# Performance work log

Measured on AMD Instinct MI355X. Metric: run time of the kernel, lower is better.

The kernel has to match this reference:

```python
import jax, jax.numpy as jnp
import numpy as np

RING_WORLD_SIZE = 4  # number of ring steps / KV sequence chunks


def _ring_flash_attention(q, k, v, ring_size):
    # q,k,v: [B, S, H, D]; non-causal full attention computed blockwise over
    # KV chunks (one per ring step) with numerically-stable online LSE merge,
    # mirroring _compact_ring_fwd + update_out_and_lse.
    B, S, H, D = q.shape
    scale = D ** (-0.5)
    chunk = S // ring_size
    out = None  # [B, S, H, D] accumulated in fp32
    lse = None  # [B, H, S] running log-sum-exp
    for step in range(ring_size):
        k_blk = jax.lax.dynamic_slice_in_dim(k, step * chunk, chunk, axis=1)
        v_blk = jax.lax.dynamic_slice_in_dim(v, step * chunk, chunk, axis=1)
        # scores: [B, H, Sq, Sk_blk]
        scores = jnp.einsum('bqhd,bkhd->bhqk', q, k_blk) * scale
        block_lse = jax.scipy.special.logsumexp(scores, axis=-1)  # [B,H,Sq]
        probs = jnp.exp(scores - block_lse[..., None])
        block_out = jnp.einsum('bhqk,bkhd->bqhd', probs, v_blk)
        if out is None:
            out, lse = block_out, block_lse
        else:
            new_lse = jnp.logaddexp(lse, block_lse)
            w_old = jnp.exp(lse - new_lse)       # [B,H,Sq]
            w_new = jnp.exp(block_lse - new_lse)
            # broadcast weights to [B,Sq,H,1]
            out = (jnp.transpose(w_old, (0, 2, 1))[..., None] * out
                   + jnp.transpose(w_new, (0, 2, 1))[..., None] * block_out)
            lse = new_lse
    return out.astype(q.dtype)


def setup_inputs() -> dict:
    key = jax.random.key(0)
    kq, kk, kv = jax.random.split(key, 3)
    shape = (1, 4096, 16, 128)
    return {
        'query': jax.random.normal(kq, shape, dtype=jnp.float32),
        'key': jax.random.normal(kk, shape, dtype=jnp.float32),
        'value': jax.random.normal(kv, shape, dtype=jnp.float32),
    }


def reference(query, key, value):
    # Ulysses all-to-all is identity on a single logical device; the ring loop
    # with lossless (error-feedback) KV compression reduces to blockwise
    # attention with online softmax merging.
    return _ring_flash_attention(query, key, value, RING_WORLD_SIZE)
```

## Files before the change

kernel.cpp:

```cpp
#include <hip/hip_runtime.h>
#include <hip/hip_bf16.h>

#define S_LEN 4096
#define NH    16
#define DD    128
#define HD    2048
#define QB    128
#define KB    64
#define NT    (S_LEN/KB)

typedef __bf16 bf16_t;
typedef bf16_t bf16x8 __attribute__((ext_vector_type(8)));
typedef float  f32x4  __attribute__((ext_vector_type(4)));

static __device__ __forceinline__ bf16x8 pack8(float4 a, float4 b, float s) {
  bf16x8 v;
  v[0]=(bf16_t)(a.x*s); v[1]=(bf16_t)(a.y*s); v[2]=(bf16_t)(a.z*s); v[3]=(bf16_t)(a.w*s);
  v[4]=(bf16_t)(b.x*s); v[5]=(bf16_t)(b.y*s); v[6]=(bf16_t)(b.z*s); v[7]=(bf16_t)(b.w*s);
  return v;
}

static __device__ __forceinline__ void gload_lds16(const void* g, void* l) {
  __builtin_amdgcn_global_load_lds((const __attribute__((address_space(1))) void*)g,
                                   (__attribute__((address_space(3))) void*)l, 16, 0, 0);
}

__global__ __launch_bounds__(256) void prep_k(const float* __restrict__ Kg,
                                              bf16_t* __restrict__ Kp) {
  const int kt = blockIdx.x, h = blockIdx.y, tid = threadIdx.x;
  __shared__ bf16_t tile[KB][DD + 8];
  #pragma unroll
  for (int it = 0; it < 8; ++it) {
    int lin4 = it*256 + tid;
    int r  = lin4 >> 5;
    int dc = (lin4 & 31) * 4;
    float4 a = *(const float4*)(Kg + (size_t)(kt*KB + r)*HD + h*DD + dc);
    tile[r][dc+0]=(bf16_t)a.x; tile[r][dc+1]=(bf16_t)a.y;
    tile[r][dc+2]=(bf16_t)a.z; tile[r][dc+3]=(bf16_t)a.w;
  }
  __syncthreads();
  bf16_t* out = Kp + (size_t)(h*NT + kt)*8192;
  #pragma unroll
  for (int it = 0; it < 4; ++it) {
    int cid = it*256 + tid;
    int f = cid >> 6, l = cid & 63;
    int b = f >> 2, c = f & 3;
    int row = b*16 + (l & 15);
    int d0  = c*32 + (l >> 4)*8;
    bf16x8 v = *(const bf16x8*)(&tile[row][d0]);
    *(bf16x8*)(out + (size_t)cid*8) = v;
  }
}

__global__ __launch_bounds__(256) void prep_v(const float* __restrict__ Vg,
                                              bf16_t* __restrict__ Vp) {
  const int kt = blockIdx.x, h = blockIdx.y, tid = threadIdx.x;
  __shared__ bf16_t tile[KB][DD + 8];
  #pragma unroll
  for (int it = 0; it < 8; ++it) {
    int lin4 = it*256 + tid;
    int r  = lin4 >> 5;
    int dc = (lin4 & 31) * 4;
    float4 a = *(const float4*)(Vg + (size_t)(kt*KB + r)*HD + h*DD + dc);
    tile[r][dc+0]=(bf16_t)a.x; tile[r][dc+1]=(bf16_t)a.y;
    tile[r][dc+2]=(bf16_t)a.z; tile[r][dc+3]=(bf16_t)a.w;
  }
  __syncthreads();
  bf16_t* out = Vp + (size_t)(h*NT + kt)*8192;
  #pragma unroll
  for (int it = 0; it < 4; ++it) {
    int cid = it*256 + tid;
    int f = cid >> 6, l = cid & 63;
    int ks = f >> 3, db = f & 7;
    int d  = db*16 + (l & 15);
    int c0 = ks*32 + (l >> 4)*8;
    bf16x8 v;
    #pragma unroll
    for (int m = 0; m < 8; ++m) {
      int c = c0 + m;
      int k = 32*(c>>5) + 16*((c>>2)&1) + 4*((c>>3)&3) + (c&3);
      v[m] = tile[k][d];
    }
    *(bf16x8*)(out + (size_t)cid*8) = v;
  }
}

__global__ __launch_bounds__(256, 2) void attn_fwd(const float* __restrict__ Qg,
                                                   const bf16_t* __restrict__ Kp,
                                                   const bf16_t* __restrict__ Vp,
                                                   float* __restrict__ Og) {
  const int phys = blockIdx.x;
  const int logical = (phys & 7) * 64 + (phys >> 3);
  const int h  = logical >> 5;
  const int qt = logical & 31;
  const int tid  = threadIdx.x;
  const int wid  = tid >> 6;
  const int lane = tid & 63;
  const int l16  = lane & 15;
  const int lg   = lane >> 4;
  const int lo16 = lane * 16;

  __shared__ alignas(16) bf16_t Ks[2][8192];
  __shared__ alignas(16) bf16_t Vt[2][8192];

  const float qs = 0.08838834764831845f * 1.4426950408889634f;
  bf16x8 qf[2][4];
  #pragma unroll
  for (int g = 0; g < 2; ++g) {
    const int qrow = qt*QB + wid*32 + g*16 + l16;
    const float* qp = Qg + (size_t)qrow*HD + h*DD + lg*8;
    #pragma unroll
    for (int c = 0; c < 4; ++c) {
      float4 a = *(const float4*)(qp + c*32);
      float4 b = *(const float4*)(qp + c*32 + 4);
      qf[g][c] = pack8(a, b, qs);
    }
  }
  bf16x8 onesf;
  #pragma unroll
  for (int j = 0; j < 8; ++j) onesf[j] = (bf16_t)1.0f;
  asm volatile("" ::: "memory");

  const int lo = tid*16;
  auto issue = [&](int kt) {
    int b = kt & 1;
    const char* kg = (const char*)(Kp + (size_t)(h*NT + kt)*8192);
    const char* vg = (const char*)(Vp + (size_t)(h*NT + kt)*8192);
    char* kl = (char*)&Ks[b][0];
    char* vl = (char*)&Vt[b][0];
    #pragma unroll
    for (int p = 0; p < 4; ++p) gload_lds16(kg + lo + p*4096, kl + lo + p*4096);
    #pragma unroll
    for (int p = 0; p < 4; ++p) gload_lds16(vg + lo + p*4096, vl + lo + p*4096);
  };

  f32x4 acc[2][8];
  f32x4 acc_l[2];
  #pragma unroll
  for (int g = 0; g < 2; ++g) {
    #pragma unroll
    for (int i = 0; i < 8; ++i) acc[g][i] = (f32x4){0.f,0.f,0.f,0.f};
    acc_l[g] = (f32x4){0.f,0.f,0.f,0.f};
  }
  float m_run[2] = {-__builtin_inff(), -__builtin_inff()};

  issue(0);
  issue(1);

  for (int kt = 0; kt < NT; ++kt) {
    if (kt == NT-1) { asm volatile("s_waitcnt vmcnt(0)" ::: "memory"); }
    else            { asm volatile("s_waitcnt vmcnt(8)" ::: "memory"); }
    __builtin_amdgcn_s_barrier();
    asm volatile("" ::: "memory");

    const int cur = kt & 1;
    const char* KsB = (const char*)&Ks[cur][0] + lo16;
    const char* VtB = (const char*)&Vt[cur][0] + lo16;

    f32x4 sc[2][4];
    #pragma unroll
    for (int g = 0; g < 2; ++g)
      #pragma unroll
      for (int b = 0; b < 4; ++b) sc[g][b] = (f32x4){0.f,0.f,0.f,0.f};
    __builtin_amdgcn_s_setprio(1);
    #pragma unroll
    for (int b = 0; b < 4; ++b) {
      #pragma unroll
      for (int c = 0; c < 4; ++c) {
        bf16x8 kb = *(const bf16x8*)(KsB + ((b*4 + c) << 10));
        sc[0][b] = __builtin_amdgcn_mfma_f32_16x16x32_bf16(kb, qf[0][c], sc[0][b], 0, 0, 0);
        sc[1][b] = __builtin_amdgcn_mfma_f32_16x16x32_bf16(kb, qf[1][c], sc[1][b], 0, 0, 0);
      }
    }
    __builtin_amdgcn_s_setprio(0);

    bf16x8 vf0[8], vf1[8];
    #pragma unroll
    for (int db = 0; db < 8; ++db) vf0[db] = *(const bf16x8*)(VtB + (db << 10));
    #pragma unroll
    for (int db = 0; db < 8; ++db) vf1[db] = *(const bf16x8*)(VtB + ((8 + db) << 10));

    bf16x8 pp[2][2];
    #pragma unroll
    for (int g = 0; g < 2; ++g) {
      float pmax;
      {
        float a0 = fmaxf(fmaxf(sc[g][0][0], sc[g][0][1]), sc[g][0][2]);
        float a1 = fmaxf(fmaxf(sc[g][0][3], sc[g][1][0]), sc[g][1][1]);
        float a2 = fmaxf(fmaxf(sc[g][1][2], sc[g][1][3]), sc[g][2][0]);
        float a3 = fmaxf(fmaxf(sc[g][2][1], sc[g][2][2]), sc[g][2][3]);
        float a4 = fmaxf(fmaxf(sc[g][3][0], sc[g][3][1]), sc[g][3][2]);
        float b0 = fmaxf(fmaxf(a0, a1), a2);
        float b1 = fmaxf(fmaxf(a3, a4), sc[g][3][3]);
        pmax = fmaxf(b0, b1);
        pmax = fmaxf(pmax, __shfl_xor(pmax, 16));
        pmax = fmaxf(pmax, __shfl_xor(pmax, 32));
      }
      if (!__all(pmax - m_run[g] <= 8.0f)) {
        float mnew  = fmaxf(m_run[g], pmax);
        float alpha = exp2f(m_run[g] - mnew);
        m_run[g] = mnew;
        #pragma unroll
        for (int i = 0; i < 8; ++i) {
          #pragma unroll
          for (int r = 0; r < 4; ++r) acc[g][i][r] *= alpha;
        }
        #pragma unroll
        for (int r = 0; r < 4; ++r) acc_l[g][r] *= alpha;
      }
      #pragma unroll
      for (int b = 0; b < 4; ++b) {
        #pragma unroll
        for (int r = 0; r < 4; ++r) {
          float p = exp2f(sc[g][b][r] - m_run[g]);
          pp[g][b >> 1][(b & 1)*4 + r] = (bf16_t)p;
        }
      }
    }

    __builtin_amdgcn_s_setprio(1);
    #pragma unroll
    for (int ks = 0; ks < 2; ++ks) {
      acc_l[0] = __builtin_amdgcn_mfma_f32_16x16x32_bf16(onesf, pp[0][ks], acc_l[0], 0, 0, 0);
      acc_l[1] = __builtin_amdgcn_mfma_f32_16x16x32_bf16(onesf, pp[1][ks], acc_l[1], 0, 0, 0);
      #pragma unroll
      for (int db = 0; db < 8; ++db) {
        bf16x8 va = ks ? vf1[db] : vf0[db];
        acc[0][db] = __builtin_amdgcn_mfma_f32_16x16x32_bf16(va, pp[0][ks], acc[0][db], 0, 0, 0);
        acc[1][db] = __builtin_amdgcn_mfma_f32_16x16x32_bf16(va, pp[1][ks], acc[1][db], 0, 0, 0);
      }
    }
    __builtin_amdgcn_s_setprio(0);

    __builtin_amdgcn_s_barrier();
    asm volatile("" ::: "memory");
    if (kt + 2 < NT) issue(kt + 2);
  }

  #pragma unroll
  for (int g = 0; g < 2; ++g) {
    const int qrow = qt*QB + wid*32 + g*16 + l16;
    const float inv = 1.0f / acc_l[g][0];
    float* op = Og + (size_t)qrow*HD + h*DD + lg*4;
    #pragma unroll
    for (int db = 0; db < 8; ++db) {
      float4 o;
      o.x = acc[g][db][0]*inv; o.y = acc[g][db][1]*inv;
      o.z = acc[g][db][2]*inv; o.w = acc[g][db][3]*inv;
      *(float4*)(op + db*16) = o;
    }
  }
}

extern "C" void kernel_launch(void* const* d_in, const int* in_sizes, int n_in,
                              void* d_out, int out_size, void* d_ws, size_t ws_size,
                              hipStream_t stream) {
  const float* Q = (const float*)d_in[0];
  const float* K = (const float*)d_in[1];
  const float* V = (const float*)d_in[2];
  float* O = (float*)d_out;
  bf16_t* Kp = (bf16_t*)d_ws;
  bf16_t* Vp = Kp + (size_t)NH*S_LEN*DD;
  prep_k<<<dim3(NT, NH), 256, 0, stream>>>(K, Kp);
  prep_v<<<dim3(NT, NH), 256, 0, stream>>>(V, Vp);
  attn_fwd<<<dim3(512), 256, 0, stream>>>(Q, Kp, Vp, O);
}
```

Baseline: 188.4 us.

## Software-pipeline QK^T of next tile with softmax and PV of current tile

Restructures the main loop so the QK^T MFMAs for tile kt+1 are computed before the softmax and PV of tile kt, with a prologue and an epilogue. The V fragments are loaded into registers before a barrier so the LDS buffer can be refilled earlier, and sched_barriers pin the ordering. The goal is to overlap the exp and softmax ALU work with matrix-core work and to issue prefetches sooner. The cost is extra live registers (scn plus 16 vf fragments) under launch_bounds(256,2), which risks spills or lower occupancy, and there are now two barriers per iteration.

```diff
diff --git a/kernel.cpp b/kernel.cpp
--- a/kernel.cpp
+++ b/kernel.cpp
@@ -84,6 +84,73 @@
     *(bf16x8*)(out + (size_t)cid*8) = v;
   }
 }
+
+#define QK_COMPUTE(DST, KSBASE)                                                  \
+  do {                                                                           \
+    _Pragma("unroll")                                                            \
+    for (int b_ = 0; b_ < 4; ++b_) {                                             \
+      _Pragma("unroll")                                                          \
+      for (int c_ = 0; c_ < 4; ++c_) {                                           \
+        bf16x8 kb_ = *(const bf16x8*)((KSBASE) + ((b_*4 + c_) << 10));           \
+        DST[0][b_] = __builtin_amdgcn_mfma_f32_16x16x32_bf16(kb_, qf[0][c_], DST[0][b_], 0, 0, 0); \
+        DST[1][b_] = __builtin_amdgcn_mfma_f32_16x16x32_bf16(kb_, qf[1][c_], DST[1][b_], 0, 0, 0); \
+      }                                                                          \
+    }                                                                            \
+  } while (0)
+
+#define SOFTMAX_PV(SC)                                                           \
+  do {                                                                           \
+    bf16x8 pp[2][2];                                                             \
+    _Pragma("unroll")                                                            \
+    for (int g = 0; g < 2; ++g) {                                                \
+      float pmax;                                                                \
+      {                                                                          \
+        float a0 = fmaxf(fmaxf(SC[g][0][0], SC[g][0][1]), SC[g][0][2]);          \
+        float a1 = fmaxf(fmaxf(SC[g][0][3], SC[g][1][0]), SC[g][1][1]);          \
+        float a2 = fmaxf(fmaxf(SC[g][1][2], SC[g][1][3]), SC[g][2][0]);          \
+        float a3 = fmaxf(fmaxf(SC[g][2][1], SC[g][2][2]), SC[g][2][3]);          \
+        float a4 = fmaxf(fmaxf(SC[g][3][0], SC[g][3][1]), SC[g][3][2]);          \
+        float b0 = fmaxf(fmaxf(a0, a1), a2);                                     \
+        float b1 = fmaxf(fmaxf(a3, a4), SC[g][3][3]);                            \
+        pmax = fmaxf(b0, b1);                                                    \
+        pmax = fmaxf(pmax, __shfl_xor(pmax, 16));                                \
+        pmax = fmaxf(pmax, __shfl_xor(pmax, 32));                                \
+      }                                                                          \
+      if (!__all(pmax - m_run[g] <= 8.0f)) {                                     \
+        float mnew  = fmaxf(m_run[g], pmax);                                     \
+        float alpha = exp2f(m_run[g] - mnew);                                    \
+        m_run[g] = mnew;                                                         \
+        _Pragma("unroll")                                                        \
+        for (int i = 0; i < 8; ++i) {                                            \
+          _Pragma("unroll")                                                      \
+          for (int r = 0; r < 4; ++r) acc[g][i][r] *= alpha;                     \
+        }                                                                        \
+        _Pragma("unroll")                                                        \
+        for (int r = 0; r < 4; ++r) acc_l[g][r] *= alpha;                        \
+      }                                                                          \
+      _Pragma("unroll")                                                          \
+      for (int b_ = 0; b_ < 4; ++b_) {                                           \
+        _Pragma("unroll")                                                        \
+        for (int r = 0; r < 4; ++r) {                                            \
+          float p = exp2f(SC[g][b_][r] - m_run[g]);                              \
+          pp[g][b_ >> 1][(b_ & 1)*4 + r] = (bf16_t)p;                            \
+        }                                                                        \
+      }                                                                          \
+    }                                                                            \
+    __builtin_amdgcn_s_setprio(1);                                               \
+    _Pragma("unroll")                                                            \
+    for (int ks = 0; ks < 2; ++ks) {                                             \
+      acc_l[0] = __builtin_amdgcn_mfma_f32_16x16x32_bf16(onesf, pp[0][ks], acc_l[0], 0, 0, 0); \
+      acc_l[1] = __builtin_amdgcn_mfma_f32_16x16x32_bf16(onesf, pp[1][ks], acc_l[1], 0, 0, 0); \
+      _Pragma("unroll")                                                          \
+      for (int db = 0; db < 8; ++db) {                                           \
+        bf16x8 va = vf[ks*8 + db];                                               \
+        acc[0][db] = __builtin_amdgcn_mfma_f32_16x16x32_bf16(va, pp[0][ks], acc[0][db], 0, 0, 0); \
+        acc[1][db] = __builtin_amdgcn_mfma_f32_16x16x32_bf16(va, pp[1][ks], acc[1][db], 0, 0, 0); \
+      }                                                                          \
+    }                                                                            \
+    __builtin_amdgcn_s_setprio(0);                                               \
+  } while (0)
 
 __global__ __launch_bounds__(256, 2) void attn_fwd(const float* __restrict__ Qg,
                                                    const bf16_t* __restrict__ Kp,
@@ -146,95 +213,63 @@
 
   issue(0);
   issue(1);
-
-  for (int kt = 0; kt < NT; ++kt) {
-    if (kt == NT-1) { asm volatile("s_waitcnt vmcnt(0)" ::: "memory"); }
-    else            { asm volatile("s_waitcnt vmcnt(8)" ::: "memory"); }
+  asm volatile("s_waitcnt vmcnt(8)" ::: "memory");
+  __builtin_amdgcn_s_barrier();
+  __builtin_amdgcn_sched_barrier(0);
+
+  f32x4 sc[2][4];
+  #pragma unroll
+  for (int g = 0; g < 2; ++g)
+    #pragma unroll
+    for (int b = 0; b < 4; ++b) sc[g][b] = (f32x4){0.f,0.f,0.f,0.f};
+  {
+    const char* KsB = (const char*)&Ks[0][0] + lo16;
+    QK_COMPUTE(sc, KsB);
+  }
+
+  for (int kt = 0; kt < NT-1; ++kt) {
+    const int cur = kt & 1;
+    bf16x8 vf[16];
+    {
+      const char* VtB = (const char*)&Vt[cur][0] + lo16;
+      #pragma unroll
+      for (int f = 0; f < 16; ++f) vf[f] = *(const bf16x8*)(VtB + (f << 10));
+    }
+    asm volatile("s_waitcnt lgkmcnt(0)" ::: "memory");
+    __builtin_amdgcn_sched_barrier(0);
     __builtin_amdgcn_s_barrier();
-    asm volatile("" ::: "memory");
-
-    const int cur = kt & 1;
-    const char* KsB = (const char*)&Ks[cur][0] + lo16;
-    const char* VtB = (const char*)&Vt[cur][0] + lo16;
-
-    f32x4 sc[2][4];
+    if (kt + 2 < NT) {
+      issue(kt + 2);
+      asm volatile("s_waitcnt vmcnt(8)" ::: "memory");
+    } else {
+      asm volatile("s_waitcnt vmcnt(0)" ::: "memory");
+    }
+    __builtin_amdgcn_s_barrier();
+    __builtin_amdgcn_sched_barrier(0);
+
+    f32x4 scn[2][4];
     #pragma unroll
     for (int g = 0; g < 2; ++g)
       #pragma unroll
-      for (int b = 0; b < 4; ++b) sc[g][b] = (f32x4){0.f,0.f,0.f,0.f};
-    __builtin_amdgcn_s_setprio(1);
-    #pragma unroll
-    for (int b = 0; b < 4; ++b) {
+      for (int b = 0; b < 4; ++b) scn[g][b] = (f32x4){0.f,0.f,0.f,0.f};
+    {
+      const char* KsB = (const char*)&Ks[cur ^ 1][0] + lo16;
+      QK_COMPUTE(scn, KsB);
+    }
+    SOFTMAX_PV(sc);
+
+    #pragma unroll
+    for (int g = 0; g < 2; ++g)
       #pragma unroll
-      for (int c = 0; c < 4; ++c) {
-        bf16x8 kb = *(const bf16x8*)(KsB + ((b*4 + c) << 10));
-        sc[0][b] = __builtin_amdgcn_mfma_f32_16x16x32_bf16(kb, qf[0][c], sc[0][b], 0, 0, 0);
-        sc[1][b] = __builtin_amdgcn_mfma_f32_16x16x32_bf16(kb, qf[1][c], sc[1][b], 0, 0, 0);
-      }
-    }
-    __builtin_amdgcn_s_setprio(0);
-
-    bf16x8 vf0[8], vf1[8];
-    #pragma unroll
-    for (int db = 0; db < 8; ++db) vf0[db] = *(const bf16x8*)(VtB + (db << 10));
-    #pragma unroll
-    for (int db = 0; db < 8; ++db) vf1[db] = *(const bf16x8*)(VtB + ((8 + db) << 10));
-
-    bf16x8 pp[2][2];
-    #pragma unroll
-    for (int g = 0; g < 2; ++g) {
-      float pmax;
-      {
-        float a0 = fmaxf(fmaxf(sc[g][0][0], sc[g][0][1]), sc[g][0][2]);
-        float a1 = fmaxf(fmaxf(sc[g][0][3], sc[g][1][0]), sc[g][1][1]);
-        float a2 = fmaxf(fmaxf(sc[g][1][2], sc[g][1][3]), sc[g][2][0]);
-        float a3 = fmaxf(fmaxf(sc[g][2][1], sc[g][2][2]), sc[g][2][3]);
-        float a4 = fmaxf(fmaxf(sc[g][3][0], sc[g][3][1]), sc[g][3][2]);
-        float b0 = fmaxf(fmaxf(a0, a1), a2);
-        float b1 = fmaxf(fmaxf(a3, a4), sc[g][3][3]);
-        pmax = fmaxf(b0, b1);
-        pmax = fmaxf(pmax, __shfl_xor(pmax, 16));
-        pmax = fmaxf(pmax, __shfl_xor(pmax, 32));
-      }
-      if (!__all(pmax - m_run[g] <= 8.0f)) {
-        float mnew  = fmaxf(m_run[g], pmax);
-        float alpha = exp2f(m_run[g] - mnew);
-        m_run[g] = mnew;
-        #pragma unroll
-        for (int i = 0; i < 8; ++i) {
-          #pragma unroll
-          for (int r = 0; r < 4; ++r) acc[g][i][r] *= alpha;
-        }
-        #pragma unroll
-        for (int r = 0; r < 4; ++r) acc_l[g][r] *= alpha;
-      }
-      #pragma unroll
-      for (int b = 0; b < 4; ++b) {
-        #pragma unroll
-        for (int r = 0; r < 4; ++r) {
-          float p = exp2f(sc[g][b][r] - m_run[g]);
-          pp[g][b >> 1][(b & 1)*4 + r] = (bf16_t)p;
-        }
-      }
-    }
-
-    __builtin_amdgcn_s_setprio(1);
-    #pragma unroll
-    for (int ks = 0; ks < 2; ++ks) {
-      acc_l[0] = __builtin_amdgcn_mfma_f32_16x16x32_bf16(onesf, pp[0][ks], acc_l[0], 0, 0, 0);
-      acc_l[1] = __builtin_amdgcn_mfma_f32_16x16x32_bf16(onesf, pp[1][ks], acc_l[1], 0, 0, 0);
-      #pragma unroll
-      for (int db = 0; db < 8; ++db) {
-        bf16x8 va = ks ? vf1[db] : vf0[db];
-        acc[0][db] = __builtin_amdgcn_mfma_f32_16x16x32_bf16(va, pp[0][ks], acc[0][db], 0, 0, 0);
-        acc[1][db] = __builtin_amdgcn_mfma_f32_16x16x32_bf16(va, pp[1][ks], acc[1][db], 0, 0, 0);
-      }
-    }
-    __builtin_amdgcn_s_setprio(0);
-
-    __builtin_amdgcn_s_barrier();
-    asm volatile("" ::: "memory");
-    if (kt + 2 < NT) issue(kt + 2);
+      for (int b = 0; b < 4; ++b) sc[g][b] = scn[g][b];
+  }
+
+  {
+    bf16x8 vf[16];
+    const char* VtB = (const char*)&Vt[(NT-1) & 1][0] + lo16;
+    #pragma unroll
+    for (int f = 0; f < 16; ++f) vf[f] = *(const bf16x8*)(VtB + (f << 10));
+    SOFTMAX_PV(sc);
   }
 
   #pragma unroll
```

Result: no change. 185.5 us (-1.5%).

## Load K tiles directly into registers and shrink query blocks to two waves

Applied to the files above, without the earlier changes.

K tiles now go straight from global memory into per-wave registers, prefetched one tile ahead, so K no longer passes through LDS. Only V stays double-buffered in LDS. The query block size is halved to 64 rows with 128-thread blocks and a 1024-block grid to raise block count and occupancy. The cost is redundant K global loads per wave, since each wave now fetches the full K tile, along with more register pressure from the 16 prefetched K fragments. The waitcnt and barrier schedule is also restructured to match.

```diff
diff --git a/kernel.cpp b/kernel.cpp
--- a/kernel.cpp
+++ b/kernel.cpp
@@ -5,7 +5,7 @@
 #define NH    16
 #define DD    128
 #define HD    2048
-#define QB    128
+#define QB    64
 #define KB    64
 #define NT    (S_LEN/KB)
 
@@ -85,14 +85,14 @@
   }
 }
 
-__global__ __launch_bounds__(256, 2) void attn_fwd(const float* __restrict__ Qg,
+__global__ __launch_bounds__(128, 2) void attn_fwd(const float* __restrict__ Qg,
                                                    const bf16_t* __restrict__ Kp,
                                                    const bf16_t* __restrict__ Vp,
                                                    float* __restrict__ Og) {
   const int phys = blockIdx.x;
-  const int logical = (phys & 7) * 64 + (phys >> 3);
-  const int h  = logical >> 5;
-  const int qt = logical & 31;
+  const int logical = (phys & 7) * 128 + (phys >> 3);
+  const int h  = logical >> 6;
+  const int qt = logical & 63;
   const int tid  = threadIdx.x;
   const int wid  = tid >> 6;
   const int lane = tid & 63;
@@ -100,7 +100,6 @@
   const int lg   = lane >> 4;
   const int lo16 = lane * 16;
 
-  __shared__ alignas(16) bf16_t Ks[2][8192];
   __shared__ alignas(16) bf16_t Vt[2][8192];
 
   const float qs = 0.08838834764831845f * 1.4426950408889634f;
@@ -121,17 +120,21 @@
   for (int j = 0; j < 8; ++j) onesf[j] = (bf16_t)1.0f;
   asm volatile("" ::: "memory");
 
+  const char* KpH = (const char*)(Kp + (size_t)h*NT*8192);
+  bf16x8 kreg[16];
+  auto issue_k = [&](int kt) {
+    const char* kg = KpH + (size_t)kt*16384 + lo16;
+    #pragma unroll
+    for (int f = 0; f < 16; ++f) kreg[f] = *(const bf16x8*)(kg + (f << 10));
+  };
+
   const int lo = tid*16;
-  auto issue = [&](int kt) {
-    int b = kt & 1;
-    const char* kg = (const char*)(Kp + (size_t)(h*NT + kt)*8192);
-    const char* vg = (const char*)(Vp + (size_t)(h*NT + kt)*8192);
-    char* kl = (char*)&Ks[b][0];
-    char* vl = (char*)&Vt[b][0];
-    #pragma unroll
-    for (int p = 0; p < 4; ++p) gload_lds16(kg + lo + p*4096, kl + lo + p*4096);
-    #pragma unroll
-    for (int p = 0; p < 4; ++p) gload_lds16(vg + lo + p*4096, vl + lo + p*4096);
+  const char* VpH = (const char*)(Vp + (size_t)h*NT*8192);
+  auto issue_v = [&](int kt) {
+    const char* vg = VpH + (size_t)kt*16384 + lo;
+    char* vl = (char*)&Vt[kt & 1][0] + lo;
+    #pragma unroll
+    for (int p = 0; p < 8; ++p) gload_lds16(vg + p*2048, vl + p*2048);
   };
 
   f32x4 acc[2][8];
@@ -144,18 +147,14 @@
   }
   float m_run[2] = {-__builtin_inff(), -__builtin_inff()};
 
-  issue(0);
-  issue(1);
+  issue_v(0);
+  issue_v(1);
+  issue_k(0);
+  asm volatile("s_waitcnt vmcnt(24)" ::: "memory");
+  __builtin_amdgcn_s_barrier();
 
   for (int kt = 0; kt < NT; ++kt) {
-    if (kt == NT-1) { asm volatile("s_waitcnt vmcnt(0)" ::: "memory"); }
-    else            { asm volatile("s_waitcnt vmcnt(8)" ::: "memory"); }
-    __builtin_amdgcn_s_barrier();
-    asm volatile("" ::: "memory");
-
     const int cur = kt & 1;
-    const char* KsB = (const char*)&Ks[cur][0] + lo16;
-    const char* VtB = (const char*)&Vt[cur][0] + lo16;
 
     f32x4 sc[2][4];
     #pragma unroll
@@ -167,18 +166,14 @@
     for (int b = 0; b < 4; ++b) {
       #pragma unroll
       for (int c = 0; c < 4; ++c) {
-        bf16x8 kb = *(const bf16x8*)(KsB + ((b*4 + c) << 10));
+        bf16x8 kb = kreg[b*4 + c];
         sc[0][b] = __builtin_amdgcn_mfma_f32_16x16x32_bf16(kb, qf[0][c], sc[0][b], 0, 0, 0);
         sc[1][b] = __builtin_amdgcn_mfma_f32_16x16x32_bf16(kb, qf[1][c], sc[1][b], 0, 0, 0);
       }
     }
     __builtin_amdgcn_s_setprio(0);
 
-    bf16x8 vf0[8], vf1[8];
-    #pragma unroll
-    for (int db = 0; db < 8; ++db) vf0[db] = *(const bf16x8*)(VtB + (db << 10));
-    #pragma unroll
-    for (int db = 0; db < 8; ++db) vf1[db] = *(const bf16x8*)(VtB + ((8 + db) << 10));
+    if (kt + 1 < NT) issue_k(kt + 1);
 
     bf16x8 pp[2][2];
     #pragma unroll
@@ -218,23 +213,30 @@
       }
     }
 
-    __builtin_amdgcn_s_setprio(1);
-    #pragma unroll
-    for (int ks = 0; ks < 2; ++ks) {
-      acc_l[0] = __builtin_amdgcn_mfma_f32_16x16x32_bf16(onesf, pp[0][ks], acc_l[0], 0, 0, 0);
-      acc_l[1] = __builtin_amdgcn_mfma_f32_16x16x32_bf16(onesf, pp[1][ks], acc_l[1], 0, 0, 0);
-      #pragma unroll
-      for (int db = 0; db < 8; ++db) {
-        bf16x8 va = ks ? vf1[db] : vf0[db];
-        acc[0][db] = __builtin_amdgcn_mfma_f32_16x16x32_bf16(va, pp[0][ks], acc[0][db], 0, 0, 0);
-        acc[1][db] = __builtin_amdgcn_mfma_f32_16x16x32_bf16(va, pp[1][ks], acc[1][db], 0, 0, 0);
-      }
-    }
-    __builtin_amdgcn_s_setprio(0);
-
+    {
+      const char* VtB = (const char*)&Vt[cur][0] + lo16;
+      __builtin_amdgcn_s_setprio(1);
+      #pragma unroll
+      for (int ks = 0; ks < 2; ++ks) {
+        acc_l[0] = __builtin_amdgcn_mfma_f32_16x16x32_bf16(onesf, pp[0][ks], acc_l[0], 0, 0, 0);
+        acc_l[1] = __builtin_amdgcn_mfma_f32_16x16x32_bf16(onesf, pp[1][ks], acc_l[1], 0, 0, 0);
+        #pragma unroll
+        for (int db = 0; db < 8; ++db) {
+          bf16x8 va = *(const bf16x8*)(VtB + ((ks*8 + db) << 10));
+          acc[0][db] = __builtin_amdgcn_mfma_f32_16x16x32_bf16(va, pp[0][ks], acc[0][db], 0, 0, 0);
+          acc[1][db] = __builtin_amdgcn_mfma_f32_16x16x32_bf16(va, pp[1][ks], acc[1][db], 0, 0, 0);
+        }
+      }
+      __builtin_amdgcn_s_setprio(0);
+    }
+
+    asm volatile("s_waitcnt lgkmcnt(0)" ::: "memory");
+    if (kt + 1 < NT) {
+      asm volatile("s_waitcnt vmcnt(16)" ::: "memory");
+    }
+    __builtin_amdgcn_sched_barrier(0);
     __builtin_amdgcn_s_barrier();
-    asm volatile("" ::: "memory");
-    if (kt + 2 < NT) issue(kt + 2);
+    if (kt + 2 < NT) issue_v(kt + 2);
   }
 
   #pragma unroll
@@ -263,5 +265,5 @@
   bf16_t* Vp = Kp + (size_t)NH*S_LEN*DD;
   prep_k<<<dim3(NT, NH), 256, 0, stream>>>(K, Kp);
   prep_v<<<dim3(NT, NH), 256, 0, stream>>>(V, Vp);
-  attn_fwd<<<dim3(512), 256, 0, stream>>>(Q, Kp, Vp, O);
-}
+  attn_fwd<<<dim3(1024), 128, 0, stream>>>(Q, Kp, Vp, O);
+}
```

After: 203.3 us. +7.9%, slower.

## Single-buffer K, stagger K/V prefetch, and raise occupancy target to three blocks

Applied to the files above, without the earlier changes.

K is now single-buffered in LDS while V stays double-buffered. The next V tile is prefetched right after the top-of-loop barrier, and the next K tile right after QK^T finishes via a second barrier. V fragments are read from LDS inside the PV MFMA loop rather than held in registers, and the cross-lane max shuffles run only when a rescale is needed. Launch bounds go from 2 to 3 blocks per CU to trade registers and LDS for occupancy. The risks are a shallower prefetch with a full vmcnt(0) wait every iteration, an extra barrier, possible spills under the tighter register budget, and no occupancy gain if the grid already supplies only two blocks per CU.

```diff
diff --git a/kernel.cpp b/kernel.cpp
--- a/kernel.cpp
+++ b/kernel.cpp
@@ -85,7 +85,7 @@
   }
 }
 
-__global__ __launch_bounds__(256, 2) void attn_fwd(const float* __restrict__ Qg,
+__global__ __launch_bounds__(256, 3) void attn_fwd(const float* __restrict__ Qg,
                                                    const bf16_t* __restrict__ Kp,
                                                    const bf16_t* __restrict__ Vp,
                                                    float* __restrict__ Og) {
@@ -100,7 +100,7 @@
   const int lg   = lane >> 4;
   const int lo16 = lane * 16;
 
-  __shared__ alignas(16) bf16_t Ks[2][8192];
+  __shared__ alignas(16) bf16_t Ks[8192];
   __shared__ alignas(16) bf16_t Vt[2][8192];
 
   const float qs = 0.08838834764831845f * 1.4426950408889634f;
@@ -122,14 +122,15 @@
   asm volatile("" ::: "memory");
 
   const int lo = tid*16;
-  auto issue = [&](int kt) {
-    int b = kt & 1;
+  auto issueK = [&](int kt) {
     const char* kg = (const char*)(Kp + (size_t)(h*NT + kt)*8192);
+    char* kl = (char*)&Ks[0];
+    #pragma unroll
+    for (int p = 0; p < 4; ++p) gload_lds16(kg + lo + p*4096, kl + lo + p*4096);
+  };
+  auto issueV = [&](int kt) {
     const char* vg = (const char*)(Vp + (size_t)(h*NT + kt)*8192);
-    char* kl = (char*)&Ks[b][0];
-    char* vl = (char*)&Vt[b][0];
-    #pragma unroll
-    for (int p = 0; p < 4; ++p) gload_lds16(kg + lo + p*4096, kl + lo + p*4096);
+    char* vl = (char*)&Vt[kt & 1][0];
     #pragma unroll
     for (int p = 0; p < 4; ++p) gload_lds16(vg + lo + p*4096, vl + lo + p*4096);
   };
@@ -144,41 +145,41 @@
   }
   float m_run[2] = {-__builtin_inff(), -__builtin_inff()};
 
-  issue(0);
-  issue(1);
+  issueK(0);
+  issueV(0);
 
   for (int kt = 0; kt < NT; ++kt) {
-    if (kt == NT-1) { asm volatile("s_waitcnt vmcnt(0)" ::: "memory"); }
-    else            { asm volatile("s_waitcnt vmcnt(8)" ::: "memory"); }
+    const int cur = kt & 1;
+    asm volatile("s_waitcnt vmcnt(0) lgkmcnt(0)" ::: "memory");
+    __builtin_amdgcn_sched_barrier(0);
     __builtin_amdgcn_s_barrier();
-    asm volatile("" ::: "memory");
-
-    const int cur = kt & 1;
-    const char* KsB = (const char*)&Ks[cur][0] + lo16;
-    const char* VtB = (const char*)&Vt[cur][0] + lo16;
+
+    if (kt + 1 < NT) issueV(kt + 1);
 
     f32x4 sc[2][4];
     #pragma unroll
     for (int g = 0; g < 2; ++g)
       #pragma unroll
       for (int b = 0; b < 4; ++b) sc[g][b] = (f32x4){0.f,0.f,0.f,0.f};
-    __builtin_amdgcn_s_setprio(1);
-    #pragma unroll
-    for (int b = 0; b < 4; ++b) {
-      #pragma unroll
-      for (int c = 0; c < 4; ++c) {
-        bf16x8 kb = *(const bf16x8*)(KsB + ((b*4 + c) << 10));
-        sc[0][b] = __builtin_amdgcn_mfma_f32_16x16x32_bf16(kb, qf[0][c], sc[0][b], 0, 0, 0);
-        sc[1][b] = __builtin_amdgcn_mfma_f32_16x16x32_bf16(kb, qf[1][c], sc[1][b], 0, 0, 0);
-      }
-    }
-    __builtin_amdgcn_s_setprio(0);
-
-    bf16x8 vf0[8], vf1[8];
-    #pragma unroll
-    for (int db = 0; db < 8; ++db) vf0[db] = *(const bf16x8*)(VtB + (db << 10));
-    #pragma unroll
-    for (int db = 0; db < 8; ++db) vf1[db] = *(const bf16x8*)(VtB + ((8 + db) << 10));
+    {
+      const char* KsB = (const char*)&Ks[0] + lo16;
+      __builtin_amdgcn_s_setprio(1);
+      #pragma unroll
+      for (int b = 0; b < 4; ++b) {
+        #pragma unroll
+        for (int c = 0; c < 4; ++c) {
+          bf16x8 kb = *(const bf16x8*)(KsB + ((b*4 + c) << 10));
+          sc[0][b] = __builtin_amdgcn_mfma_f32_16x16x32_bf16(kb, qf[0][c], sc[0][b], 0, 0, 0);
+          sc[1][b] = __builtin_amdgcn_mfma_f32_16x16x32_bf16(kb, qf[1][c], sc[1][b], 0, 0, 0);
+        }
+      }
+      __builtin_amdgcn_s_setprio(0);
+    }
+
+    asm volatile("s_waitcnt lgkmcnt(0)" ::: "memory");
+    __builtin_amdgcn_sched_barrier(0);
+    __builtin_amdgcn_s_barrier();
+    if (kt + 1 < NT) issueK(kt + 1);
 
     bf16x8 pp[2][2];
     #pragma unroll
@@ -193,10 +194,10 @@
         float b0 = fmaxf(fmaxf(a0, a1), a2);
         float b1 = fmaxf(fmaxf(a3, a4), sc[g][3][3]);
         pmax = fmaxf(b0, b1);
+      }
+      if (!__all(pmax - m_run[g] <= 8.0f)) {
         pmax = fmaxf(pmax, __shfl_xor(pmax, 16));
         pmax = fmaxf(pmax, __shfl_xor(pmax, 32));
-      }
-      if (!__all(pmax - m_run[g] <= 8.0f)) {
         float mnew  = fmaxf(m_run[g], pmax);
         float alpha = exp2f(m_run[g] - mnew);
         m_run[g] = mnew;
@@ -218,23 +219,22 @@
       }
     }
 
-    __builtin_amdgcn_s_setprio(1);
-    #pragma unroll
-    for (int ks = 0; ks < 2; ++ks) {
-      acc_l[0] = __builtin_amdgcn_mfma_f32_16x16x32_bf16(onesf, pp[0][ks], acc_l[0], 0, 0, 0);
-      acc_l[1] = __builtin_amdgcn_mfma_f32_16x16x32_bf16(onesf, pp[1][ks], acc_l[1], 0, 0, 0);
-      #pragma unroll
-      for (int db = 0; db < 8; ++db) {
-        bf16x8 va = ks ? vf1[db] : vf0[db];
-        acc[0][db] = __builtin_amdgcn_mfma_f32_16x16x32_bf16(va, pp[0][ks], acc[0][db], 0, 0, 0);
-        acc[1][db] = __builtin_amdgcn_mfma_f32_16x16x32_bf16(va, pp[1][ks], acc[1][db], 0, 0, 0);
-      }
-    }
-    __builtin_amdgcn_s_setprio(0);
-
-    __builtin_amdgcn_s_barrier();
-    asm volatile("" ::: "memory");
-    if (kt + 2 < NT) issue(kt + 2);
+    {
+      const char* VtB = (const char*)&Vt[cur][0] + lo16;
+      __builtin_amdgcn_s_setprio(1);
+      #pragma unroll
+      for (int ks = 0; ks < 2; ++ks) {
+        acc_l[0] = __builtin_amdgcn_mfma_f32_16x16x32_bf16(onesf, pp[0][ks], acc_l[0], 0, 0, 0);
+        acc_l[1] = __builtin_amdgcn_mfma_f32_16x16x32_bf16(onesf, pp[1][ks], acc_l[1], 0, 0, 0);
+        #pragma unroll
+        for (int db = 0; db < 8; ++db) {
+          bf16x8 va = *(const bf16x8*)(VtB + ((ks*8 + db) << 10));
+          acc[0][db] = __builtin_amdgcn_mfma_f32_16x16x32_bf16(va, pp[0][ks], acc[0][db], 0, 0, 0);
+          acc[1][db] = __builtin_amdgcn_mfma_f32_16x16x32_bf16(va, pp[1][ks], acc[1][db], 0, 0, 0);
+        }
+      }
+      __builtin_amdgcn_s_setprio(0);
+    }
   }
 
   #pragma unroll
```

After: 189.0 us. No clear change (+0.3%).
